# Kernel tuning notes

Measured on AMD Instinct MI355X. Metric: run time of the kernel, lower is better.

## Reference

```python
import jax, jax.numpy as jnp
import numpy as np

D_MODEL = 1024
H = 16
D_K = D_MODEL // H
SEQ = 4096
SIM_WEIGHT = 1.0


def setup_inputs() -> dict:
    key = jax.random.key(0)
    ks = jax.random.split(key, 10)
    s = 1.0 / np.sqrt(D_MODEL)
    return {
        "x": jax.random.normal(ks[0], (SEQ, D_MODEL), dtype=jnp.float32),
        "similarity_matrix": jax.random.normal(ks[1], (SEQ, SEQ), dtype=jnp.float32),
        "w_q": jax.random.normal(ks[2], (D_MODEL, D_MODEL), dtype=jnp.float32) * s,
        "b_q": jnp.zeros((D_MODEL,), dtype=jnp.float32),
        "w_k": jax.random.normal(ks[3], (D_MODEL, D_MODEL), dtype=jnp.float32) * s,
        "b_k": jnp.zeros((D_MODEL,), dtype=jnp.float32),
        "w_v": jax.random.normal(ks[4], (D_MODEL, D_MODEL), dtype=jnp.float32) * s,
        "b_v": jnp.zeros((D_MODEL,), dtype=jnp.float32),
        "w_o": jax.random.normal(ks[5], (D_MODEL, D_MODEL), dtype=jnp.float32) * s,
        "b_o": jnp.zeros((D_MODEL,), dtype=jnp.float32),
    }


def reference(x, similarity_matrix, w_q, b_q, w_k, b_k, w_v, b_v, w_o, b_o):
    # x: [S, D]; project and split heads -> [H, S, d_k]
    q = (x @ w_q.T + b_q).reshape(SEQ, H, D_K).transpose(1, 0, 2)
    k = (x @ w_k.T + b_k).reshape(SEQ, H, D_K).transpose(1, 0, 2)
    v = (x @ w_v.T + b_v).reshape(SEQ, H, D_K).transpose(1, 0, 2)
    # scores: [H, S, S]; additive similarity bias broadcast over heads
    scores = jnp.einsum("hsd,htd->hst", q, k) / jnp.sqrt(jnp.float32(D_K))
    scores = scores + similarity_matrix[None, :, :] * SIM_WEIGHT
    attn = jax.nn.softmax(scores, axis=-1)
    out = jnp.einsum("hst,htd->hsd", attn, v)  # [H, S, d_k]
    out = out.transpose(1, 0, 2).reshape(SEQ, D_MODEL)
    return out @ w_o.T + b_o
```

## Files before the change

### kernel.cpp

```cpp
#include <hip/hip_runtime.h>
#include <hip/hip_bf16.h>

typedef __hip_bfloat16 bf16;
typedef __attribute__((ext_vector_type(8))) short short8;
typedef __attribute__((ext_vector_type(4))) float f32x4;

#define SEQ    4096
#define DMODEL 1024
#define NHEAD  16
#define DKH    64

#define LSTRIDE 72
#define PSTRIDE 72

__device__ __forceinline__ float ldf(const float* p, size_t i) { return p[i]; }
__device__ __forceinline__ float ldf(const bf16*  p, size_t i) { return __bfloat162float(p[i]); }
__device__ __forceinline__ void stf(float* p, size_t i, float v) { p[i] = v; }
__device__ __forceinline__ void stf(bf16*  p, size_t i, float v) { p[i] = __float2bfloat16(v); }

__device__ __forceinline__ short f2bs(float v) {
    bf16 b = __float2bfloat16(v);
    return *(short*)&b;
}

__device__ __forceinline__ short8 lda8(const bf16* p, size_t i) {
    return *(const short8*)(p + i);
}
__device__ __forceinline__ short8 lda8(const float* p, size_t i) {
    float4 a = *(const float4*)(p + i);
    float4 b = *(const float4*)(p + i + 4);
    short8 r;
    r[0] = f2bs(a.x); r[1] = f2bs(a.y); r[2] = f2bs(a.z); r[3] = f2bs(a.w);
    r[4] = f2bs(b.x); r[5] = f2bs(b.y); r[6] = f2bs(b.z); r[7] = f2bs(b.w);
    return r;
}

__device__ __forceinline__ void g2l16(const void* g, void* l) {
    __builtin_amdgcn_global_load_lds(
        (const __attribute__((address_space(1))) unsigned int*)g,
        (__attribute__((address_space(3))) unsigned int*)l, 16, 0, 0);
}

__global__ void detect_dtype(const unsigned short* __restrict__ x, int* __restrict__ flag) {
    int lane = threadIdx.x;
    int cnt = 0;
    for (int i = lane; i < 512; i += 64) {
        int e = (x[i] >> 7) & 0xFF;
        cnt += (e >= 100 && e <= 140) ? 1 : 0;
    }
    #pragma unroll
    for (int off = 32; off; off >>= 1) cnt += __shfl_xor(cnt, off, 64);
    if (lane == 0) *flag = (cnt >= 400) ? 1 : 0;
}

template <typename TC>
__device__ void gemm_dma_body(const bf16* __restrict__ A, const bf16* __restrict__ B,
                              const bf16* __restrict__ bias, TC* __restrict__ C,
                              int m0, int n0, int M, int N, int K, bool transc,
                              short* As, short* Bs) {
    const int tid = threadIdx.x;
    const int w = tid >> 6, lane = tid & 63, q = lane >> 4, c = lane & 15;
    const int mb = 64 * (w & 1), nb = 64 * (w >> 1);

    f32x4 acc[4][4] = {};

    for (int k0 = 0; k0 < K; k0 += 64) {
        __syncthreads();
        #pragma unroll
        for (int i = 0; i < 4; ++i) {
            int p = i * 256 + tid;
            int row = p >> 3, pc = p & 7, gc = pc ^ (row & 7);
            g2l16(A + (size_t)(m0 + row) * K + k0 + gc * 8, As + (size_t)p * 8);
            g2l16(B + (size_t)(n0 + row) * K + k0 + gc * 8, Bs + (size_t)p * 8);
        }
        __syncthreads();
        #pragma unroll
        for (int kh = 0; kh < 2; ++kh) {
            short8 af[4], bfr[4];
            #pragma unroll
            for (int i = 0; i < 4; ++i) {
                int row = mb + i * 16 + c;
                af[i] = *(const short8*)&As[row * 64 + (((kh * 4 + q) ^ (row & 7)) << 3)];
            }
            #pragma unroll
            for (int j = 0; j < 4; ++j) {
                int row = nb + j * 16 + c;
                bfr[j] = *(const short8*)&Bs[row * 64 + (((kh * 4 + q) ^ (row & 7)) << 3)];
            }
            #pragma unroll
            for (int i = 0; i < 4; ++i)
                #pragma unroll
                for (int j = 0; j < 4; ++j)
                    acc[i][j] = __builtin_amdgcn_mfma_f32_16x16x32_bf16(af[i], bfr[j], acc[i][j], 0, 0, 0);
        }
    }

    #pragma unroll
    for (int j = 0; j < 4; ++j) {
        int n = n0 + nb + j * 16 + c;
        float bj = __bfloat162float(bias[n]);
        #pragma unroll
        for (int i = 0; i < 4; ++i) {
            if (transc) {
                short4 pk;
                pk.x = f2bs(acc[i][j][0] + bj);
                pk.y = f2bs(acc[i][j][1] + bj);
                pk.z = f2bs(acc[i][j][2] + bj);
                pk.w = f2bs(acc[i][j][3] + bj);
                int m = m0 + mb + i * 16 + q * 4;
                *(short4*)&((bf16*)C)[(size_t)n * M + m] = pk;
            } else {
                #pragma unroll
                for (int t = 0; t < 4; ++t) {
                    int m = m0 + mb + i * 16 + q * 4 + t;
                    stf(C, (size_t)m * N + n, acc[i][j][t] + bj);
                }
            }
        }
    }
}

template <typename TC>
__device__ void gemm_dma64_body(const bf16* __restrict__ A, const bf16* __restrict__ B,
                                const bf16* __restrict__ bias, TC* __restrict__ C,
                                int m0, int n0, int M, int N, int K,
                                short* As, short* Bs) {
    const int tid = threadIdx.x;
    const int w = tid >> 6, lane = tid & 63, q = lane >> 4, c = lane & 15;
    const int nb = 32 * w;

    f32x4 acc[4][2] = {};

    for (int k0 = 0; k0 < K; k0 += 64) {
        __syncthreads();
        #pragma unroll
        for (int i = 0; i < 2; ++i) {
            int p = i * 256 + tid;
            int row = p >> 3, pc = p & 7, gc = pc ^ (row & 7);
            g2l16(A + (size_t)(m0 + row) * K + k0 + gc * 8, As + (size_t)p * 8);
        }
        #pragma unroll
        for (int i = 0; i < 4; ++i) {
            int p = i * 256 + tid;
            int row = p >> 3, pc = p & 7, gc = pc ^ (row & 7);
            g2l16(B + (size_t)(n0 + row) * K + k0 + gc * 8, Bs + (size_t)p * 8);
        }
        __syncthreads();
        #pragma unroll
        for (int kh = 0; kh < 2; ++kh) {
            short8 af[4], bfr[2];
            #pragma unroll
            for (int i = 0; i < 4; ++i) {
                int row = i * 16 + c;
                af[i] = *(const short8*)&As[row * 64 + (((kh * 4 + q) ^ (row & 7)) << 3)];
            }
            #pragma unroll
            for (int j = 0; j < 2; ++j) {
                int row = nb + j * 16 + c;
                bfr[j] = *(const short8*)&Bs[row * 64 + (((kh * 4 + q) ^ (row & 7)) << 3)];
            }
            #pragma unroll
            for (int i = 0; i < 4; ++i)
                #pragma unroll
                for (int j = 0; j < 2; ++j)
                    acc[i][j] = __builtin_amdgcn_mfma_f32_16x16x32_bf16(af[i], bfr[j], acc[i][j], 0, 0, 0);
        }
    }

    #pragma unroll
    for (int j = 0; j < 2; ++j) {
        int n = n0 + nb + j * 16 + c;
        float bj = __bfloat162float(bias[n]);
        #pragma unroll
        for (int i = 0; i < 4; ++i)
            #pragma unroll
            for (int t = 0; t < 4; ++t) {
                int m = m0 + i * 16 + q * 4 + t;
                stf(C, (size_t)m * N + n, acc[i][j][t] + bj);
            }
    }
}

template <typename TA, typename TB, typename TC>
__device__ void gemm_legacy_body(const TA* __restrict__ A, const TB* __restrict__ B,
                                 const TB* __restrict__ bias, TC* __restrict__ C,
                                 int m0, int n0, int M, int N, int K, bool transc,
                                 short* As, short* Bs) {
    const int tid = threadIdx.x;
    const int w = tid >> 6, lane = tid & 63, q = lane >> 4, c = lane & 15;
    const int mb = 64 * (w & 1), nb = 64 * (w >> 1);

    f32x4 acc[4][4] = {};

    for (int k0 = 0; k0 < K; k0 += 64) {
        __syncthreads();
        #pragma unroll
        for (int i = 0; i < 4; ++i) {
            int ch = tid + 256 * i;
            int r = ch >> 3, c8 = (ch & 7) * 8;
            *(short8*)&As[r * LSTRIDE + c8] = lda8(A, (size_t)(m0 + r) * K + k0 + c8);
            *(short8*)&Bs[r * LSTRIDE + c8] = lda8(B, (size_t)(n0 + r) * K + k0 + c8);
        }
        __syncthreads();
        #pragma unroll
        for (int kh = 0; kh < 2; ++kh) {
            const int kk = kh * 32 + q * 8;
            short8 af[4], bfr[4];
            #pragma unroll
            for (int i = 0; i < 4; ++i)
                af[i] = *(const short8*)&As[(mb + i * 16 + c) * LSTRIDE + kk];
            #pragma unroll
            for (int j = 0; j < 4; ++j)
                bfr[j] = *(const short8*)&Bs[(nb + j * 16 + c) * LSTRIDE + kk];
            #pragma unroll
            for (int i = 0; i < 4; ++i)
                #pragma unroll
                for (int j = 0; j < 4; ++j)
                    acc[i][j] = __builtin_amdgcn_mfma_f32_16x16x32_bf16(af[i], bfr[j], acc[i][j], 0, 0, 0);
        }
    }

    #pragma unroll
    for (int j = 0; j < 4; ++j) {
        int n = n0 + nb + j * 16 + c;
        float bj = ldf(bias, (size_t)n);
        #pragma unroll
        for (int i = 0; i < 4; ++i) {
            if (transc) {
                short4 pk;
                pk.x = f2bs(acc[i][j][0] + bj);
                pk.y = f2bs(acc[i][j][1] + bj);
                pk.z = f2bs(acc[i][j][2] + bj);
                pk.w = f2bs(acc[i][j][3] + bj);
                int m = m0 + mb + i * 16 + q * 4;
                *(short4*)&((bf16*)C)[(size_t)n * M + m] = pk;
            } else {
                #pragma unroll
                for (int t = 0; t < 4; ++t) {
                    int m = m0 + mb + i * 16 + q * 4 + t;
                    stf(C, (size_t)m * N + n, acc[i][j][t] + bj);
                }
            }
        }
    }
}

__global__ __launch_bounds__(256)
void gemm_qkv(const void* __restrict__ x,
              const void* __restrict__ wq, const void* __restrict__ bq,
              const void* __restrict__ wk, const void* __restrict__ bk,
              const void* __restrict__ wv, const void* __restrict__ bv,
              bf16* __restrict__ Q, bf16* __restrict__ K, bf16* __restrict__ Vt,
              const int* __restrict__ flag) {
    __shared__ __align__(16) short As[128 * LSTRIDE];
    __shared__ __align__(16) short Bs[128 * LSTRIDE];
    const int sel = blockIdx.y >> 3;
    const int m0 = blockIdx.x * 128, n0 = (blockIdx.y & 7) * 128;
    const void* B  = (sel == 0) ? wq : (sel == 1) ? wk : wv;
    const void* bi = (sel == 0) ? bq : (sel == 1) ? bk : bv;
    bf16* C        = (sel == 0) ? Q  : (sel == 1) ? K  : Vt;
    const bool tr = (sel == 2);
    if (*flag)
        gemm_dma_body<bf16>((const bf16*)x, (const bf16*)B, (const bf16*)bi, C,
                            m0, n0, SEQ, DMODEL, DMODEL, tr, As, Bs);
    else
        gemm_legacy_body<float, float, bf16>((const float*)x, (const float*)B, (const float*)bi, C,
                                             m0, n0, SEQ, DMODEL, DMODEL, tr, As, Bs);
}

__global__ __launch_bounds__(256)
void gemm_out_k(const bf16* __restrict__ A, const void* __restrict__ B,
                const void* __restrict__ bias, void* __restrict__ C,
                const int* __restrict__ flag, int M, int N, int K) {
    __shared__ __align__(16) short As[128 * LSTRIDE];
    __shared__ __align__(16) short Bs[128 * LSTRIDE];
    if (*flag) {
        gemm_dma64_body<bf16>(A, (const bf16*)B, (const bf16*)bias, (bf16*)C,
                              blockIdx.x * 64, blockIdx.y * 128, M, N, K, As, Bs);
    } else {
        if (blockIdx.x >= (unsigned)(M / 128)) return;
        gemm_legacy_body<bf16, float, float>(A, (const float*)B, (const float*)bias, (float*)C,
                                             blockIdx.x * 128, blockIdx.y * 128, M, N, K, false, As, Bs);
    }
}

template <typename TS, bool SPLIT>
__device__ void flash_body(const bf16* __restrict__ Q, const bf16* __restrict__ Kg,
                           const bf16* __restrict__ VtG, const TS* __restrict__ sim,
                           bf16* __restrict__ O, float* __restrict__ Opart,
                           float* __restrict__ Lpart, short* Ps, int t0, int nt) {
    const int tid = threadIdx.x;
    const int w = tid >> 6, lane = tid & 63, q = lane >> 4, c = lane & 15;
    const int q0 = blockIdx.x * 128, hd = blockIdx.y * DKH;
    const int kz = blockIdx.z;
    const int r0 = q0 + w * 32;

    short8 aq[2][2];
    #pragma unroll
    for (int m = 0; m < 2; ++m)
        #pragma unroll
        for (int kc = 0; kc < 2; ++kc)
            aq[m][kc] = *(const short8*)&Q[(size_t)(r0 + m * 16 + c) * DMODEL + hd + kc * 32 + q * 8];

    const TS* simp[2][4];
    #pragma unroll
    for (int m = 0; m < 2; ++m)
        #pragma unroll
        for (int i = 0; i < 4; ++i)
            simp[m][i] = sim + (size_t)(r0 + m * 16 + q * 4 + i) * SEQ + c;

    f32x4 accO[2][4] = {};
    float Lp[2][4] = {};

    for (int t = t0; t < t0 + nt; ++t) {
        const int k0 = t * 64;

        short8 bk[4][2];
        #pragma unroll
        for (int f = 0; f < 4; ++f)
            #pragma unroll
            for (int kc = 0; kc < 2; ++kc)
                bk[f][kc] = *(const short8*)&Kg[(size_t)(k0 + f * 16 + c) * DMODEL + hd + kc * 32 + q * 8];

        f32x4 sfr[2][4];
        #pragma unroll
        for (int m = 0; m < 2; ++m)
            #pragma unroll
            for (int f = 0; f < 4; ++f) {
                f32x4 a = {};
                a = __builtin_amdgcn_mfma_f32_16x16x32_bf16(aq[m][0], bk[f][0], a, 0, 0, 0);
                a = __builtin_amdgcn_mfma_f32_16x16x32_bf16(aq[m][1], bk[f][1], a, 0, 0, 0);
                sfr[m][f] = a;
            }

        #pragma unroll
        for (int m = 0; m < 2; ++m)
            #pragma unroll
            for (int f = 0; f < 4; ++f)
                #pragma unroll
                for (int i = 0; i < 4; ++i) {
                    float s = sfr[m][f][i] * 0.125f + ldf(simp[m][i], (size_t)k0 + f * 16);
                    float p = __expf(s);
                    Lp[m][i] += p;
                    Ps[(w * 32 + m * 16 + q * 4 + i) * PSTRIDE + f * 16 + c] = f2bs(p);
                }

        short8 bv[4][2];
        #pragma unroll
        for (int f = 0; f < 4; ++f)
            #pragma unroll
            for (int kc = 0; kc < 2; ++kc)
                bv[f][kc] = *(const short8*)&VtG[(size_t)(hd + f * 16 + c) * SEQ + k0 + kc * 32 + q * 8];

        short8 ap[2][2];
        #pragma unroll
        for (int m = 0; m < 2; ++m)
            #pragma unroll
            for (int kc = 0; kc < 2; ++kc)
                ap[m][kc] = *(const short8*)&Ps[(w * 32 + m * 16 + c) * PSTRIDE + kc * 32 + q * 8];

        #pragma unroll
        for (int m = 0; m < 2; ++m)
            #pragma unroll
            for (int f = 0; f < 4; ++f) {
                accO[m][f] = __builtin_amdgcn_mfma_f32_16x16x32_bf16(ap[m][0], bv[f][0], accO[m][f], 0, 0, 0);
                accO[m][f] = __builtin_amdgcn_mfma_f32_16x16x32_bf16(ap[m][1], bv[f][1], accO[m][f], 0, 0, 0);
            }
    }

    #pragma unroll
    for (int off = 1; off < 16; off <<= 1)
        #pragma unroll
        for (int m = 0; m < 2; ++m)
            #pragma unroll
            for (int i = 0; i < 4; ++i)
                Lp[m][i] += __shfl_xor(Lp[m][i], off, 64);

    if (SPLIT) {
        #pragma unroll
        for (int m = 0; m < 2; ++m)
            #pragma unroll
            for (int i = 0; i < 4; ++i) {
                int gr = r0 + m * 16 + q * 4 + i;
                if (c == 0)
                    Lpart[((size_t)kz * NHEAD + blockIdx.y) * SEQ + gr] = Lp[m][i];
                #pragma unroll
                for (int f = 0; f < 4; ++f)
                    Opart[((size_t)kz * SEQ + gr) * DMODEL + hd + f * 16 + c] = accO[m][f][i];
            }
    } else {
        #pragma unroll
        for (int m = 0; m < 2; ++m)
            #pragma unroll
            for (int i = 0; i < 4; ++i) {
                float inv = 1.f / Lp[m][i];
                int gr = r0 + m * 16 + q * 4 + i;
                #pragma unroll
                for (int f = 0; f < 4; ++f)
                    O[(size_t)gr * DMODEL + hd + f * 16 + c] = __float2bfloat16(accO[m][f][i] * inv);
            }
    }
}

__global__ __launch_bounds__(256)
void flash_split(const bf16* __restrict__ Q, const bf16* __restrict__ K,
                 const bf16* __restrict__ Vt, const void* __restrict__ sim,
                 float* __restrict__ Opart, float* __restrict__ Lpart,
                 const int* __restrict__ flag, int t0mul, int nt) {
    __shared__ __align__(16) short Ps[128 * PSTRIDE];
    const int t0 = blockIdx.z * t0mul;
    if (*flag)
        flash_body<bf16, true>(Q, K, Vt, (const bf16*)sim, nullptr, Opart, Lpart, Ps, t0, nt);
    else
        flash_body<float, true>(Q, K, Vt, (const float*)sim, nullptr, Opart, Lpart, Ps, t0, nt);
}

__global__ __launch_bounds__(256)
void flash_ns(const bf16* __restrict__ Q, const bf16* __restrict__ K,
              const bf16* __restrict__ Vt, const void* __restrict__ sim,
              bf16* __restrict__ O, const int* __restrict__ flag) {
    __shared__ __align__(16) short Ps[128 * PSTRIDE];
    if (*flag)
        flash_body<bf16, false>(Q, K, Vt, (const bf16*)sim, O, nullptr, nullptr, Ps, 0, SEQ / 64);
    else
        flash_body<float, false>(Q, K, Vt, (const float*)sim, O, nullptr, nullptr, Ps, 0, SEQ / 64);
}

__global__ __launch_bounds__(256)
void combine_k(const float* __restrict__ Opart, const float* __restrict__ Lpart,
               bf16* __restrict__ O) {
    size_t idx = (size_t)blockIdx.x * 256 + threadIdx.x;
    size_t base = idx * 4;
    int row = (int)(base >> 10);
    int d = (int)(base & 1023);
    int h = d >> 6;
    const float4 a = *(const float4*)&Opart[base];
    const float4 b = *(const float4*)&Opart[(size_t)SEQ * DMODEL + base];
    float L = Lpart[(size_t)h * SEQ + row] + Lpart[(size_t)(NHEAD + h) * SEQ + row];
    float inv = 1.f / L;
    short4 pk;
    pk.x = f2bs((a.x + b.x) * inv);
    pk.y = f2bs((a.y + b.y) * inv);
    pk.z = f2bs((a.z + b.z) * inv);
    pk.w = f2bs((a.w + b.w) * inv);
    *(short4*)&O[base] = pk;
}

extern "C" void kernel_launch(void* const* d_in, const int* in_sizes, int n_in,
                              void* d_out, int out_size, void* d_ws, size_t ws_size,
                              hipStream_t stream) {
    int* flagw = (int*)d_ws;
    const int* flag = (const int*)d_ws;
    bf16* Q  = (bf16*)((char*)d_ws + 256);
    bf16* K  = Q + (size_t)SEQ * DMODEL;
    bf16* Vt = K + (size_t)SEQ * DMODEL;
    bf16* O  = Vt + (size_t)SEQ * DMODEL;
    float* Lpart = (float*)(O + (size_t)SEQ * DMODEL);
    float* Opart = Lpart + 2 * (size_t)NHEAD * SEQ;

    const size_t need = 256 + 4 * (size_t)SEQ * DMODEL * sizeof(bf16)
                      + 2 * (size_t)NHEAD * SEQ * sizeof(float)
                      + 2 * (size_t)SEQ * DMODEL * sizeof(float);
    const bool split = (ws_size >= need);

    detect_dtype<<<1, 64, 0, stream>>>((const unsigned short*)d_in[0], flagw);

    dim3 blk(256);
    gemm_qkv<<<dim3(SEQ / 128, 24), blk, 0, stream>>>(
        d_in[0], d_in[2], d_in[3], d_in[4], d_in[5], d_in[6], d_in[7], Q, K, Vt, flag);

    if (split) {
        flash_split<<<dim3(SEQ / 128, NHEAD, 2), blk, 0, stream>>>(
            Q, K, Vt, d_in[1], Opart, Lpart, flag, SEQ / 128, SEQ / 128);
        combine_k<<<dim3(SEQ * DMODEL / 1024), blk, 0, stream>>>(Opart, Lpart, O);
    } else {
        flash_ns<<<dim3(SEQ / 128, NHEAD), blk, 0, stream>>>(Q, K, Vt, d_in[1], O, flag);
    }

    gemm_out_k<<<dim3(SEQ / 64, DMODEL / 128), blk, 0, stream>>>(
        O, d_in[8], d_in[9], d_out, flag, SEQ, DMODEL, DMODEL);
}
```

Before: 504.6 us.

## Transpose flash attention to keep P in registers and prefetch K and sim

The flash kernel now computes S^T = K·Q^T, so the score fragment layout matches the B-operand layout for the P·V MFMA. The shared-memory round trip for P and its LDS traffic go away. The 1/sqrt(dk) scale is folded into the Q projection epilogue, and the similarity bias is loaded as the MFMA accumulator initial value. K and similarity tiles are double-buffered in registers one tile ahead. This raises register pressure and may reduce occupancy.

```diff
diff --git a/kernel.cpp b/kernel.cpp
--- a/kernel.cpp
+++ b/kernel.cpp
@@ -11,7 +11,6 @@
 #define DKH    64
 
 #define LSTRIDE 72
-#define PSTRIDE 72
 
 __device__ __forceinline__ float ldf(const float* p, size_t i) { return p[i]; }
 __device__ __forceinline__ float ldf(const bf16*  p, size_t i) { return __bfloat162float(p[i]); }
@@ -21,6 +20,10 @@
 __device__ __forceinline__ short f2bs(float v) {
     bf16 b = __float2bfloat16(v);
     return *(short*)&b;
+}
+__device__ __forceinline__ float bs2f(short s) {
+    unsigned u = ((unsigned)(unsigned short)s) << 16;
+    return __uint_as_float(u);
 }
 
 __device__ __forceinline__ short8 lda8(const bf16* p, size_t i) {
@@ -53,10 +56,23 @@
     if (lane == 0) *flag = (cnt >= 400) ? 1 : 0;
 }
 
+template <typename TS> struct SimT;
+template <> struct SimT<bf16>  { using V = short4; };
+template <> struct SimT<float> { using V = float4; };
+
+__device__ __forceinline__ f32x4 cvt4(short4 s) {
+    f32x4 r;
+    r[0] = bs2f(s.x); r[1] = bs2f(s.y); r[2] = bs2f(s.z); r[3] = bs2f(s.w);
+    return r;
+}
+__device__ __forceinline__ f32x4 cvt4(float4 v) {
+    f32x4 r; r[0] = v.x; r[1] = v.y; r[2] = v.z; r[3] = v.w; return r;
+}
+
 template <typename TC>
 __device__ void gemm_dma_body(const bf16* __restrict__ A, const bf16* __restrict__ B,
                               const bf16* __restrict__ bias, TC* __restrict__ C,
-                              int m0, int n0, int M, int N, int K, bool transc,
+                              int m0, int n0, int M, int N, int K, bool transc, float cscale,
                               short* As, short* Bs) {
     const int tid = threadIdx.x;
     const int w = tid >> 6, lane = tid & 63, q = lane >> 4, c = lane & 15;
@@ -103,17 +119,17 @@
         for (int i = 0; i < 4; ++i) {
             if (transc) {
                 short4 pk;
-                pk.x = f2bs(acc[i][j][0] + bj);
-                pk.y = f2bs(acc[i][j][1] + bj);
-                pk.z = f2bs(acc[i][j][2] + bj);
-                pk.w = f2bs(acc[i][j][3] + bj);
+                pk.x = f2bs((acc[i][j][0] + bj) * cscale);
+                pk.y = f2bs((acc[i][j][1] + bj) * cscale);
+                pk.z = f2bs((acc[i][j][2] + bj) * cscale);
+                pk.w = f2bs((acc[i][j][3] + bj) * cscale);
                 int m = m0 + mb + i * 16 + q * 4;
                 *(short4*)&((bf16*)C)[(size_t)n * M + m] = pk;
             } else {
                 #pragma unroll
                 for (int t = 0; t < 4; ++t) {
                     int m = m0 + mb + i * 16 + q * 4 + t;
-                    stf(C, (size_t)m * N + n, acc[i][j][t] + bj);
+                    stf(C, (size_t)m * N + n, (acc[i][j][t] + bj) * cscale);
                 }
             }
         }
@@ -184,7 +200,7 @@
 template <typename TA, typename TB, typename TC>
 __device__ void gemm_legacy_body(const TA* __restrict__ A, const TB* __restrict__ B,
                                  const TB* __restrict__ bias, TC* __restrict__ C,
-                                 int m0, int n0, int M, int N, int K, bool transc,
+                                 int m0, int n0, int M, int N, int K, bool transc, float cscale,
                                  short* As, short* Bs) {
     const int tid = threadIdx.x;
     const int w = tid >> 6, lane = tid & 63, q = lane >> 4, c = lane & 15;
@@ -228,17 +244,17 @@
         for (int i = 0; i < 4; ++i) {
             if (transc) {
                 short4 pk;
-                pk.x = f2bs(acc[i][j][0] + bj);
-                pk.y = f2bs(acc[i][j][1] + bj);
-                pk.z = f2bs(acc[i][j][2] + bj);
-                pk.w = f2bs(acc[i][j][3] + bj);
+                pk.x = f2bs((acc[i][j][0] + bj) * cscale);
+                pk.y = f2bs((acc[i][j][1] + bj) * cscale);
+                pk.z = f2bs((acc[i][j][2] + bj) * cscale);
+                pk.w = f2bs((acc[i][j][3] + bj) * cscale);
                 int m = m0 + mb + i * 16 + q * 4;
                 *(short4*)&((bf16*)C)[(size_t)n * M + m] = pk;
             } else {
                 #pragma unroll
                 for (int t = 0; t < 4; ++t) {
                     int m = m0 + mb + i * 16 + q * 4 + t;
-                    stf(C, (size_t)m * N + n, acc[i][j][t] + bj);
+                    stf(C, (size_t)m * N + n, (acc[i][j][t] + bj) * cscale);
                 }
             }
         }
@@ -260,12 +276,13 @@
     const void* bi = (sel == 0) ? bq : (sel == 1) ? bk : bv;
     bf16* C        = (sel == 0) ? Q  : (sel == 1) ? K  : Vt;
     const bool tr = (sel == 2);
+    const float cs = (sel == 0) ? 0.125f : 1.0f;
     if (*flag)
         gemm_dma_body<bf16>((const bf16*)x, (const bf16*)B, (const bf16*)bi, C,
-                            m0, n0, SEQ, DMODEL, DMODEL, tr, As, Bs);
+                            m0, n0, SEQ, DMODEL, DMODEL, tr, cs, As, Bs);
     else
         gemm_legacy_body<float, float, bf16>((const float*)x, (const float*)B, (const float*)bi, C,
-                                             m0, n0, SEQ, DMODEL, DMODEL, tr, As, Bs);
+                                             m0, n0, SEQ, DMODEL, DMODEL, tr, cs, As, Bs);
 }
 
 __global__ __launch_bounds__(256)
@@ -280,125 +297,147 @@
     } else {
         if (blockIdx.x >= (unsigned)(M / 128)) return;
         gemm_legacy_body<bf16, float, float>(A, (const float*)B, (const float*)bias, (float*)C,
-                                             blockIdx.x * 128, blockIdx.y * 128, M, N, K, false, As, Bs);
-    }
-}
-
-template <typename TS, bool SPLIT>
-__device__ void flash_body(const bf16* __restrict__ Q, const bf16* __restrict__ Kg,
+                                             blockIdx.x * 128, blockIdx.y * 128, M, N, K, false, 1.0f, As, Bs);
+    }
+}
+
+template <typename TS, bool SPLIT, int NT>
+__device__ void flash_body(const bf16* __restrict__ Qg, const bf16* __restrict__ Kg,
                            const bf16* __restrict__ VtG, const TS* __restrict__ sim,
                            bf16* __restrict__ O, float* __restrict__ Opart,
-                           float* __restrict__ Lpart, short* Ps, int t0, int nt) {
+                           float* __restrict__ Lpart) {
+    using SV = typename SimT<TS>::V;
     const int tid = threadIdx.x;
     const int w = tid >> 6, lane = tid & 63, q = lane >> 4, c = lane & 15;
-    const int q0 = blockIdx.x * 128, hd = blockIdx.y * DKH;
-    const int kz = blockIdx.z;
-    const int r0 = q0 + w * 32;
-
-    short8 aq[2][2];
+    const int hd = blockIdx.y * DKH;
+    const int kz = SPLIT ? blockIdx.z : 0;
+    const int t0 = kz * NT;
+    const int r0 = blockIdx.x * 128 + w * 32;
+
+    short8 qf[2][2];
     #pragma unroll
     for (int m = 0; m < 2; ++m)
         #pragma unroll
         for (int kc = 0; kc < 2; ++kc)
-            aq[m][kc] = *(const short8*)&Q[(size_t)(r0 + m * 16 + c) * DMODEL + hd + kc * 32 + q * 8];
-
-    const TS* simp[2][4];
+            qf[m][kc] = *(const short8*)&Qg[(size_t)(r0 + m * 16 + c) * DMODEL + hd + kc * 32 + q * 8];
+
+    short8 Ka[2][4][2];
+    SV     sb[2][2][4];
+
+    #pragma unroll
+    for (int f = 0; f < 4; ++f)
+        #pragma unroll
+        for (int kc = 0; kc < 2; ++kc)
+            Ka[0][f][kc] = *(const short8*)&Kg[(size_t)(t0 * 64 + f * 16 + c) * DMODEL + hd + kc * 32 + q * 8];
     #pragma unroll
     for (int m = 0; m < 2; ++m)
         #pragma unroll
-        for (int i = 0; i < 4; ++i)
-            simp[m][i] = sim + (size_t)(r0 + m * 16 + q * 4 + i) * SEQ + c;
-
-    f32x4 accO[2][4] = {};
-    float Lp[2][4] = {};
-
-    for (int t = t0; t < t0 + nt; ++t) {
-        const int k0 = t * 64;
-
-        short8 bk[4][2];
-        #pragma unroll
         for (int f = 0; f < 4; ++f)
-            #pragma unroll
-            for (int kc = 0; kc < 2; ++kc)
-                bk[f][kc] = *(const short8*)&Kg[(size_t)(k0 + f * 16 + c) * DMODEL + hd + kc * 32 + q * 8];
-
-        f32x4 sfr[2][4];
-        #pragma unroll
-        for (int m = 0; m < 2; ++m)
-            #pragma unroll
-            for (int f = 0; f < 4; ++f) {
-                f32x4 a = {};
-                a = __builtin_amdgcn_mfma_f32_16x16x32_bf16(aq[m][0], bk[f][0], a, 0, 0, 0);
-                a = __builtin_amdgcn_mfma_f32_16x16x32_bf16(aq[m][1], bk[f][1], a, 0, 0, 0);
-                sfr[m][f] = a;
-            }
-
-        #pragma unroll
-        for (int m = 0; m < 2; ++m)
+            sb[0][m][f] = *(const SV*)&sim[(size_t)(r0 + m * 16 + c) * SEQ + t0 * 64 + f * 16 + q * 4];
+
+    f32x4 accOT[4][2] = {};
+    float Lp[2] = {};
+
+    for (int tp = 0; tp < NT; tp += 2) {
+        #pragma unroll
+        for (int sub = 0; sub < 2; ++sub) {
+            const int cur = sub, nxt = sub ^ 1;
+            const int t = tp + sub;
+            const int k0 = (t0 + t) * 64;
+            const int tn = (t + 1 < NT) ? t + 1 : 0;
+            const int kn = (t0 + tn) * 64;
+
             #pragma unroll
             for (int f = 0; f < 4; ++f)
                 #pragma unroll
-                for (int i = 0; i < 4; ++i) {
-                    float s = sfr[m][f][i] * 0.125f + ldf(simp[m][i], (size_t)k0 + f * 16);
-                    float p = __expf(s);
-                    Lp[m][i] += p;
-                    Ps[(w * 32 + m * 16 + q * 4 + i) * PSTRIDE + f * 16 + c] = f2bs(p);
+                for (int kc = 0; kc < 2; ++kc)
+                    Ka[nxt][f][kc] = *(const short8*)&Kg[(size_t)(kn + f * 16 + c) * DMODEL + hd + kc * 32 + q * 8];
+            #pragma unroll
+            for (int m = 0; m < 2; ++m)
+                #pragma unroll
+                for (int f = 0; f < 4; ++f)
+                    sb[nxt][m][f] = *(const SV*)&sim[(size_t)(r0 + m * 16 + c) * SEQ + kn + f * 16 + q * 4];
+
+            short4 vt0[4][2], vt1[4][2];
+            #pragma unroll
+            for (int fp = 0; fp < 4; ++fp)
+                #pragma unroll
+                for (int cc = 0; cc < 2; ++cc) {
+                    const bf16* vb = &VtG[(size_t)(hd + fp * 16 + c) * SEQ + k0 + cc * 32 + 4 * q];
+                    vt0[fp][cc] = *(const short4*)vb;
+                    vt1[fp][cc] = *(const short4*)(vb + 16);
                 }
 
-        short8 bv[4][2];
-        #pragma unroll
-        for (int f = 0; f < 4; ++f)
-            #pragma unroll
-            for (int kc = 0; kc < 2; ++kc)
-                bv[f][kc] = *(const short8*)&VtG[(size_t)(hd + f * 16 + c) * SEQ + k0 + kc * 32 + q * 8];
-
-        short8 ap[2][2];
-        #pragma unroll
-        for (int m = 0; m < 2; ++m)
-            #pragma unroll
-            for (int kc = 0; kc < 2; ++kc)
-                ap[m][kc] = *(const short8*)&Ps[(w * 32 + m * 16 + c) * PSTRIDE + kc * 32 + q * 8];
-
-        #pragma unroll
-        for (int m = 0; m < 2; ++m)
-            #pragma unroll
-            for (int f = 0; f < 4; ++f) {
-                accO[m][f] = __builtin_amdgcn_mfma_f32_16x16x32_bf16(ap[m][0], bv[f][0], accO[m][f], 0, 0, 0);
-                accO[m][f] = __builtin_amdgcn_mfma_f32_16x16x32_bf16(ap[m][1], bv[f][1], accO[m][f], 0, 0, 0);
-            }
-    }
-
-    #pragma unroll
-    for (int off = 1; off < 16; off <<= 1)
-        #pragma unroll
-        for (int m = 0; m < 2; ++m)
-            #pragma unroll
-            for (int i = 0; i < 4; ++i)
-                Lp[m][i] += __shfl_xor(Lp[m][i], off, 64);
-
-    if (SPLIT) {
-        #pragma unroll
-        for (int m = 0; m < 2; ++m)
-            #pragma unroll
-            for (int i = 0; i < 4; ++i) {
-                int gr = r0 + m * 16 + q * 4 + i;
-                if (c == 0)
-                    Lpart[((size_t)kz * NHEAD + blockIdx.y) * SEQ + gr] = Lp[m][i];
-                #pragma unroll
-                for (int f = 0; f < 4; ++f)
-                    Opart[((size_t)kz * SEQ + gr) * DMODEL + hd + f * 16 + c] = accO[m][f][i];
-            }
-    } else {
-        #pragma unroll
-        for (int m = 0; m < 2; ++m)
-            #pragma unroll
-            for (int i = 0; i < 4; ++i) {
-                float inv = 1.f / Lp[m][i];
-                int gr = r0 + m * 16 + q * 4 + i;
-                #pragma unroll
-                for (int f = 0; f < 4; ++f)
-                    O[(size_t)gr * DMODEL + hd + f * 16 + c] = __float2bfloat16(accO[m][f][i] * inv);
-            }
+            f32x4 st[4][2];
+            #pragma unroll
+            for (int f = 0; f < 4; ++f)
+                #pragma unroll
+                for (int m = 0; m < 2; ++m) {
+                    f32x4 a = cvt4(sb[cur][m][f]);
+                    a = __builtin_amdgcn_mfma_f32_16x16x32_bf16(Ka[cur][f][0], qf[m][0], a, 0, 0, 0);
+                    a = __builtin_amdgcn_mfma_f32_16x16x32_bf16(Ka[cur][f][1], qf[m][1], a, 0, 0, 0);
+                    st[f][m] = a;
+                }
+
+            short8 bp[2][2];
+            #pragma unroll
+            for (int m = 0; m < 2; ++m)
+                #pragma unroll
+                for (int cc = 0; cc < 2; ++cc) {
+                    #pragma unroll
+                    for (int h = 0; h < 2; ++h) {
+                        const int f = 2 * cc + h;
+                        #pragma unroll
+                        for (int i = 0; i < 4; ++i) {
+                            float p = __expf(st[f][m][i]);
+                            Lp[m] += p;
+                            bp[m][cc][4 * h + i] = f2bs(p);
+                        }
+                    }
+                }
+
+            #pragma unroll
+            for (int cc = 0; cc < 2; ++cc)
+                #pragma unroll
+                for (int fp = 0; fp < 4; ++fp) {
+                    short8 av;
+                    #pragma unroll
+                    for (int i = 0; i < 4; ++i) { av[i] = ((short*)&vt0[fp][cc])[i]; av[4 + i] = ((short*)&vt1[fp][cc])[i]; }
+                    #pragma unroll
+                    for (int m = 0; m < 2; ++m)
+                        accOT[fp][m] = __builtin_amdgcn_mfma_f32_16x16x32_bf16(av, bp[m][cc], accOT[fp][m], 0, 0, 0);
+                }
+        }
+    }
+
+    #pragma unroll
+    for (int m = 0; m < 2; ++m) {
+        Lp[m] += __shfl_xor(Lp[m], 16, 64);
+        Lp[m] += __shfl_xor(Lp[m], 32, 64);
+    }
+
+    #pragma unroll
+    for (int m = 0; m < 2; ++m) {
+        const int row = r0 + m * 16 + c;
+        if (SPLIT) {
+            if (q == 0)
+                Lpart[((size_t)kz * NHEAD + blockIdx.y) * SEQ + row] = Lp[m];
+            #pragma unroll
+            for (int fp = 0; fp < 4; ++fp)
+                *(float4*)&Opart[((size_t)kz * SEQ + row) * DMODEL + hd + fp * 16 + q * 4] =
+                    *(float4*)&accOT[fp][m];
+        } else {
+            float inv = 1.f / Lp[m];
+            #pragma unroll
+            for (int fp = 0; fp < 4; ++fp) {
+                short4 pk;
+                pk.x = f2bs(accOT[fp][m][0] * inv);
+                pk.y = f2bs(accOT[fp][m][1] * inv);
+                pk.z = f2bs(accOT[fp][m][2] * inv);
+                pk.w = f2bs(accOT[fp][m][3] * inv);
+                *(short4*)&O[(size_t)row * DMODEL + hd + fp * 16 + q * 4] = pk;
+            }
+        }
     }
 }
 
@@ -406,24 +445,21 @@
 void flash_split(const bf16* __restrict__ Q, const bf16* __restrict__ K,
                  const bf16* __restrict__ Vt, const void* __restrict__ sim,
                  float* __restrict__ Opart, float* __restrict__ Lpart,
-                 const int* __restrict__ flag, int t0mul, int nt) {
-    __shared__ __align__(16) short Ps[128 * PSTRIDE];
-    const int t0 = blockIdx.z * t0mul;
+                 const int* __restrict__ flag) {
     if (*flag)
-        flash_body<bf16, true>(Q, K, Vt, (const bf16*)sim, nullptr, Opart, Lpart, Ps, t0, nt);
+        flash_body<bf16, true, SEQ / 128>(Q, K, Vt, (const bf16*)sim, nullptr, Opart, Lpart);
     else
-        flash_body<float, true>(Q, K, Vt, (const float*)sim, nullptr, Opart, Lpart, Ps, t0, nt);
+        flash_body<float, true, SEQ / 128>(Q, K, Vt, (const float*)sim, nullptr, Opart, Lpart);
 }
 
 __global__ __launch_bounds__(256)
 void flash_ns(const bf16* __restrict__ Q, const bf16* __restrict__ K,
               const bf16* __restrict__ Vt, const void* __restrict__ sim,
               bf16* __restrict__ O, const int* __restrict__ flag) {
-    __shared__ __align__(16) short Ps[128 * PSTRIDE];
     if (*flag)
-        flash_body<bf16, false>(Q, K, Vt, (const bf16*)sim, O, nullptr, nullptr, Ps, 0, SEQ / 64);
+        flash_body<bf16, false, SEQ / 64>(Q, K, Vt, (const bf16*)sim, O, nullptr, nullptr);
     else
-        flash_body<float, false>(Q, K, Vt, (const float*)sim, O, nullptr, nullptr, Ps, 0, SEQ / 64);
+        flash_body<float, false, SEQ / 64>(Q, K, Vt, (const float*)sim, O, nullptr, nullptr);
 }
 
 __global__ __launch_bounds__(256)
@@ -471,7 +507,7 @@
 
     if (split) {
         flash_split<<<dim3(SEQ / 128, NHEAD, 2), blk, 0, stream>>>(
-            Q, K, Vt, d_in[1], Opart, Lpart, flag, SEQ / 128, SEQ / 128);
+            Q, K, Vt, d_in[1], Opart, Lpart, flag);
         combine_k<<<dim3(SEQ * DMODEL / 1024), blk, 0, stream>>>(Opart, Lpart, O);
     } else {
         flash_ns<<<dim3(SEQ / 128, NHEAD), blk, 0, stream>>>(Q, K, Vt, d_in[1], O, flag);
```

Result: slower. 759.1 us (+50.4%).
